# Kernel tuning notes

Measured on AMD Instinct MI355X. Metric: run time of the kernel, lower is better.

The kernel has to match this reference:

```python
import jax, jax.numpy as jnp
import numpy as np
from jax import lax

DIM = 256
NUM_HEADS = 8
HEAD_DIM = DIM // NUM_HEADS  # 32
SCALE = HEAD_DIM ** -0.5
KERNEL_SIZES = [5, 7, 9]
DILATIONS = [1, 2, 3]
# 'favor_small' allocation: weights ~ 1/k^2 over remain=num_heads-num_ranges=5
# -> extra=[3,2,0] -> heads_per_range = [4, 3, 1]
HEADS_PER_RANGE = [4, 3, 1]
B, H, W = 2, 64, 64


def setup_inputs() -> dict:
    key = jax.random.key(0)
    ks = jax.random.split(key, 9)
    d = {"x": jax.random.normal(ks[0], (B, DIM, H, W), jnp.float32)}
    for i in range(3):
        d[f"qkv_w{i}"] = jax.random.normal(ks[1 + 2 * i], (3 * DIM, DIM), jnp.float32) * 0.02
        d[f"qkv_b{i}"] = jnp.zeros((3 * DIM,), jnp.float32)
    d["proj_w"] = jax.random.normal(ks[7], (DIM, DIM), jnp.float32) * 0.02
    d["proj_b"] = jnp.zeros((DIM,), jnp.float32)
    return d


def _unfold(x, ksz, dil, h, hd):
    # x: (B, h*hd, H, W) -> (B, h, hd, L, H*W), zero-padded like F.unfold
    b, _, hh, ww = x.shape
    p = (ksz // 2) * dil
    patches = lax.conv_general_dilated_patches(
        x, (ksz, ksz), (1, 1), [(p, p), (p, p)], rhs_dilation=(dil, dil)
    )  # (B, h*hd*L, H, W), channel-major ordering matches F.unfold
    return patches.reshape(b, h, hd, ksz * ksz, hh * ww)


def _forward(x, qkv_params, proj_w, proj_b):
    b, c, hh, ww = x.shape
    hw = hh * ww
    outs = []
    hs = 0
    for i in range(len(KERNEL_SIZES)):
        w_i, b_i = qkv_params[i]
        # 1x1 conv -> qkv
        qkv = jnp.einsum('bchw,oc->bohw', x, w_i) + b_i[None, :, None, None]
        q, k, v = jnp.split(qkv, 3, axis=1)
        h_i = HEADS_PER_RANGE[i]
        he = hs + h_i
        # slice this range's heads
        q_r = q.reshape(b, NUM_HEADS, HEAD_DIM, hh, ww)[:, hs:he]
        k_r = k.reshape(b, NUM_HEADS, HEAD_DIM, hh, ww)[:, hs:he]
        v_r = v.reshape(b, NUM_HEADS, HEAD_DIM, hh, ww)[:, hs:he]
        ksz, dil = KERNEL_SIZES[i], DILATIONS[i]
        k_nb = _unfold(k_r.reshape(b, h_i * HEAD_DIM, hh, ww), ksz, dil, h_i, HEAD_DIM)
        v_nb = _unfold(v_r.reshape(b, h_i * HEAD_DIM, hh, ww), ksz, dil, h_i, HEAD_DIM)
        q_flat = q_r.reshape(b, h_i, HEAD_DIM, hw) * SCALE
        logits = jnp.einsum('bhdp,bhdlp->bhlp', q_flat, k_nb)  # (B, h_i, L, HW)
        attn = jax.nn.softmax(logits, axis=2)
        out_i = jnp.einsum('bhlp,bhdlp->bhdp', attn, v_nb)  # (B, h_i, d, HW)
        outs.append(out_i)
        hs = he
    out = jnp.concatenate(outs, axis=1).reshape(b, c, hh, ww)
    out = jnp.einsum('bchw,oc->bohw', out, proj_w) + proj_b[None, :, None, None]
    return out


def reference(x, qkv_w0, qkv_b0, qkv_w1, qkv_b1, qkv_w2, qkv_b2, proj_w, proj_b):
    qkv_params = [(qkv_w0, qkv_b0), (qkv_w1, qkv_b1), (qkv_w2, qkv_b2)]
    return _forward(x, qkv_params, proj_w, proj_b)
```

## Files before the change

kernel.cpp:

```cpp
#include <hip/hip_runtime.h>
#include <hip/hip_bf16.h>
#include <stdint.h>
#include <stddef.h>

typedef short bf16x8 __attribute__((ext_vector_type(8)));
typedef short s16x4 __attribute__((ext_vector_type(4)));
typedef float f32x4 __attribute__((ext_vector_type(4)));

#define HW 4096
#define WDIM 64

__device__ __forceinline__ short f2bf(float f) {
  union { __hip_bfloat16 b; short s; } u;
  u.b = __float2bfloat16(f);
  return u.s;
}
__device__ __forceinline__ float bf2f(short s) {
  union { unsigned u; float f; } u;
  u.u = ((unsigned)(unsigned short)s) << 16;
  return u.f;
}

__global__ void prep_weights(const float* __restrict__ w0, const float* __restrict__ w1,
                             const float* __restrict__ w2, const float* __restrict__ b0,
                             const float* __restrict__ b1, const float* __restrict__ b2,
                             const float* __restrict__ pw,
                             short* __restrict__ Wh, short* __restrict__ Wl,
                             short* __restrict__ Ph, short* __restrict__ Pl,
                             float* __restrict__ bias_sel) {
  int idx = blockIdx.x * 256 + threadIdx.x;
  if (idx < 768 * 256) {
    int j = idx >> 8;
    int h = (j & 255) >> 5;
    const float* w = (h < 4) ? w0 : ((h < 7) ? w1 : w2);
    float v = w[idx];
    short hi = f2bf(v);
    Wh[idx] = hi;
    Wl[idx] = f2bf(v - bf2f(hi));
  } else if (idx < 768 * 256 + 256 * 256) {
    int k = idx - 768 * 256;
    float v = pw[k];
    short hi = f2bf(v);
    Ph[k] = hi;
    Pl[k] = f2bf(v - bf2f(hi));
  } else if (idx < 768 * 256 + 256 * 256 + 768) {
    int j = idx - (768 * 256 + 256 * 256);
    int h = (j & 255) >> 5;
    const float* bb = (h < 4) ? b0 : ((h < 7) ? b1 : b2);
    bias_sel[j] = bb[j];
  }
}

__global__ void transpose_x(const float* __restrict__ x, short* __restrict__ XTh,
                            short* __restrict__ XTl) {
  __shared__ float tile[32][33];
  int b = blockIdx.z;
  int p0 = blockIdx.x * 32, c0 = blockIdx.y * 32;
  int tx = threadIdx.x, ty = threadIdx.y;
  const float* xb = x + (size_t)b * 256 * HW;
  #pragma unroll
  for (int i = 0; i < 32; i += 8)
    tile[ty + i][tx] = xb[(size_t)(c0 + ty + i) * HW + p0 + tx];
  __syncthreads();
  size_t ob = (size_t)b * HW * 256;
  #pragma unroll
  for (int i = 0; i < 32; i += 8) {
    float v = tile[tx][ty + i];
    short hi = f2bf(v);
    size_t o = ob + (size_t)(p0 + ty + i) * 256 + c0 + tx;
    XTh[o] = hi;
    XTl[o] = f2bf(v - bf2f(hi));
  }
}

template <int BM, int BN, int OUT>
__global__ __launch_bounds__(256) void gemm_split(
    const short* __restrict__ Ah, const short* __restrict__ Al,
    const short* __restrict__ Bh, const short* __restrict__ Bl,
    const float* __restrict__ bias, float* __restrict__ C, int M) {
  constexpr int LD = 40;
  constexpr int AL = BM / 64, BL = BN / 64;
  constexpr int WM = BM / 2, WN = BN / 2;
  constexpr int MR = WM / 16, NR = WN / 16;
  __shared__ short Ash[BM * LD], Asl[BM * LD], Bsh[BN * LD], Bsl[BN * LD];
  int tid = threadIdx.x;
  int b = blockIdx.z;
  size_t aoff = (size_t)blockIdx.y * BM * 256;
  size_t boff = (size_t)b * HW * 256 + (size_t)blockIdx.x * BN * 256;
  int lane = tid & 63, wid = tid >> 6;
  int wm = wid >> 1, wn = wid & 1;
  int il = lane & 15, kg = lane >> 4;
  f32x4 acc[MR][NR] = {};
  int row_s = tid >> 2;
  int kk_s = (tid & 3) * 8;

  for (int kt = 0; kt < 256; kt += 32) {
    bf16x8 rah[AL], ral[AL], rbh[BL], rbl[BL];
    #pragma unroll
    for (int i = 0; i < AL; ++i) {
      size_t g = aoff + (size_t)(row_s + 64 * i) * 256 + kt + kk_s;
      rah[i] = *(const bf16x8*)&Ah[g];
      ral[i] = *(const bf16x8*)&Al[g];
    }
    #pragma unroll
    for (int i = 0; i < BL; ++i) {
      size_t g = boff + (size_t)(row_s + 64 * i) * 256 + kt + kk_s;
      rbh[i] = *(const bf16x8*)&Bh[g];
      rbl[i] = *(const bf16x8*)&Bl[g];
    }
    __syncthreads();
    #pragma unroll
    for (int i = 0; i < AL; ++i) {
      *(bf16x8*)&Ash[(row_s + 64 * i) * LD + kk_s] = rah[i];
      *(bf16x8*)&Asl[(row_s + 64 * i) * LD + kk_s] = ral[i];
    }
    #pragma unroll
    for (int i = 0; i < BL; ++i) {
      *(bf16x8*)&Bsh[(row_s + 64 * i) * LD + kk_s] = rbh[i];
      *(bf16x8*)&Bsl[(row_s + 64 * i) * LD + kk_s] = rbl[i];
    }
    __syncthreads();
    bf16x8 afh[MR], afl[MR], bfh[NR], bfl[NR];
    #pragma unroll
    for (int mr = 0; mr < MR; ++mr) {
      int r = (wm * WM + mr * 16 + il) * LD + kg * 8;
      afh[mr] = *(bf16x8*)&Ash[r];
      afl[mr] = *(bf16x8*)&Asl[r];
    }
    #pragma unroll
    for (int nr = 0; nr < NR; ++nr) {
      int r = (wn * WN + nr * 16 + il) * LD + kg * 8;
      bfh[nr] = *(bf16x8*)&Bsh[r];
      bfl[nr] = *(bf16x8*)&Bsl[r];
    }
    #pragma unroll
    for (int mr = 0; mr < MR; ++mr)
      #pragma unroll
      for (int nr = 0; nr < NR; ++nr) {
        acc[mr][nr] = __builtin_amdgcn_mfma_f32_16x16x32_bf16(afh[mr], bfh[nr], acc[mr][nr], 0, 0, 0);
        acc[mr][nr] = __builtin_amdgcn_mfma_f32_16x16x32_bf16(afh[mr], bfl[nr], acc[mr][nr], 0, 0, 0);
        acc[mr][nr] = __builtin_amdgcn_mfma_f32_16x16x32_bf16(afl[mr], bfh[nr], acc[mr][nr], 0, 0, 0);
      }
  }

  int m0 = blockIdx.y * BM, n0 = blockIdx.x * BN;
  #pragma unroll
  for (int mr = 0; mr < MR; ++mr) {
    #pragma unroll
    for (int nr = 0; nr < NR; ++nr) {
      int grow0 = m0 + wm * WM + mr * 16 + kg * 4;
      int gcol = n0 + wn * WN + nr * 16 + il;
      if (OUT == 0) {
        int t = grow0 >> 8, h = (grow0 >> 5) & 7, d0 = grow0 & 31;
        size_t base = (((size_t)(b * 3 + t) * 8 + h) << 17) + ((size_t)gcol << 5) + d0;
        f32x4 vv;
        #pragma unroll
        for (int r = 0; r < 4; ++r) vv[r] = acc[mr][nr][r] + bias[grow0 + r];
        *(f32x4*)&C[base] = vv;
      } else {
        size_t cbase = (size_t)b * M * HW;
        #pragma unroll
        for (int r = 0; r < 4; ++r)
          C[cbase + (size_t)(grow0 + r) * HW + gcol] = acc[mr][nr][r] + bias[grow0 + r];
      }
    }
  }
}

template <int KSZ, int DIL>
__device__ __forceinline__ void attn_wave(const float* __restrict__ qkvt,
                                          short* __restrict__ Yh, short* __restrict__ Yl,
                                          int b, int hq, int p0, int lane) {
  constexpr int R = KSZ / 2;
  const float SCALE = 0.17677669529663687f;
  int pl = lane & 7;
  int dq = lane >> 3;
  int p = p0 + pl;
  const float* qp = qkvt + (((size_t)(b * 24 + hq)) << 17) + ((size_t)p << 5) + dq * 4;
  const float* kb = qkvt + (((size_t)(b * 24 + 8 + hq)) << 17) + dq * 4;
  const float* vb = qkvt + (((size_t)(b * 24 + 16 + hq)) << 17) + dq * 4;

  f32x4 q = *(const f32x4*)qp;
  #pragma unroll
  for (int j = 0; j < 4; ++j) q[j] *= SCALE;

  f32x4 acc = {0.f, 0.f, 0.f, 0.f};
  float denom = 0.f;
  int y = p >> 6, x = p & 63;

  #pragma unroll
  for (int dy = -R; dy <= R; ++dy) {
    #pragma unroll
    for (int dx = -R; dx <= R; ++dx) {
      int ny = y + dy * DIL;
      int nx = x + dx * DIL;
      bool valid = ((unsigned)ny < WDIM) & ((unsigned)nx < WDIM);
      int pp = valid ? (ny * WDIM + nx) : p;
      f32x4 kk = *(const f32x4*)(kb + ((size_t)pp << 5));
      f32x4 vv = *(const f32x4*)(vb + ((size_t)pp << 5));
      float s = q[0] * kk[0] + q[1] * kk[1] + q[2] * kk[2] + q[3] * kk[3];
      s += __shfl_xor(s, 8);
      s += __shfl_xor(s, 16);
      s += __shfl_xor(s, 32);
      float e = __expf(valid ? s : 0.0f);
      denom += e;
      float en = valid ? e : 0.0f;
      #pragma unroll
      for (int j = 0; j < 4; ++j) acc[j] += en * vv[j];
    }
  }

  float inv = 1.0f / denom;
  size_t yo = ((size_t)b * HW + p) * 256 + hq * 32 + dq * 4;
  s16x4 oh, ol;
  #pragma unroll
  for (int j = 0; j < 4; ++j) {
    float v = acc[j] * inv;
    short hi = f2bf(v);
    oh[j] = hi;
    ol[j] = f2bf(v - bf2f(hi));
  }
  *(s16x4*)&Yh[yo] = oh;
  *(s16x4*)&Yl[yo] = ol;
}

__global__ __launch_bounds__(256, 8) void attn_all(const float* __restrict__ qkvt,
                                                   short* __restrict__ Yh,
                                                   short* __restrict__ Yl) {
  int tid = threadIdx.x;
  int lane = tid & 63, wave = tid >> 6;
  int gw = blockIdx.x * 4 + wave;
  if (gw < 4096) {
    int tile = gw & 511;
    int t2 = gw >> 9;
    int b = t2 & 1, h = t2 >> 1;
    attn_wave<5, 1>(qkvt, Yh, Yl, b, h, tile * 8, lane);
  } else if (gw < 7168) {
    int s = gw - 4096;
    int tile = s & 511;
    int t2 = s >> 9;
    int b = t2 & 1, h = 4 + (t2 >> 1);
    attn_wave<7, 2>(qkvt, Yh, Yl, b, h, tile * 8, lane);
  } else {
    int s = gw - 7168;
    int tile = s & 511;
    int b = s >> 9;
    attn_wave<9, 3>(qkvt, Yh, Yl, b, 7, tile * 8, lane);
  }
}

extern "C" void kernel_launch(void* const* d_in, const int* in_sizes, int n_in,
                              void* d_out, int out_size, void* d_ws, size_t ws_size,
                              hipStream_t stream) {
  const float* x  = (const float*)d_in[0];
  const float* w0 = (const float*)d_in[1];
  const float* b0 = (const float*)d_in[2];
  const float* w1 = (const float*)d_in[3];
  const float* b1 = (const float*)d_in[4];
  const float* w2 = (const float*)d_in[5];
  const float* b2 = (const float*)d_in[6];
  const float* pw = (const float*)d_in[7];
  const float* pb = (const float*)d_in[8];

  char* ws = (char*)d_ws;
  float* qkvt = (float*)ws; ws += (size_t)2 * 768 * HW * 4;
  short* XTh = (short*)ws;  ws += (size_t)2 * HW * 256 * 2;
  short* XTl = (short*)ws;  ws += (size_t)2 * HW * 256 * 2;
  short* Yh  = (short*)ws;  ws += (size_t)2 * HW * 256 * 2;
  short* Yl  = (short*)ws;  ws += (size_t)2 * HW * 256 * 2;
  short* Wh  = (short*)ws;  ws += (size_t)768 * 256 * 2;
  short* Wl  = (short*)ws;  ws += (size_t)768 * 256 * 2;
  short* Ph  = (short*)ws;  ws += (size_t)256 * 256 * 2;
  short* Pl  = (short*)ws;  ws += (size_t)256 * 256 * 2;
  float* bsel= (float*)ws;  ws += 4096;

  prep_weights<<<1027, 256, 0, stream>>>(w0, w1, w2, b0, b1, b2, pw, Wh, Wl, Ph, Pl, bsel);
  transpose_x<<<dim3(128, 8, 2), dim3(32, 8), 0, stream>>>(x, XTh, XTl);
  gemm_split<64, 128, 0><<<dim3(32, 12, 2), 256, 0, stream>>>(Wh, Wl, XTh, XTl, bsel, qkvt, 768);
  attn_all<<<2048, 256, 0, stream>>>(qkvt, Yh, Yl);
  gemm_split<64, 64, 1><<<dim3(64, 4, 2), 256, 0, stream>>>(Ph, Pl, Yh, Yl, pb, (float*)d_out, 256);
}
```

Before: 198.0 us.

## Batch neighbor loads in groups of four and remap blocks to XCDs per head

The attention inner loop now issues the K/V loads for four neighbors before computing their scores and accumulating, so more memory requests are in flight per wave. Blocks are also remapped so that each XCD (blockIdx mod 8) handles the whole spatial range of one (batch, head) pair. Neighboring tiles of the same head then share that XCD's L2 cache. The cost is higher register pressure from holding four K/V vectors at once. The mapping assumes 2048 blocks and 8 XCDs, and leaves a stray unused label in the code.

After: 243.4 us. 23.0% more time.

```diff
diff --git a/kernel.cpp b/kernel.cpp
--- a/kernel.cpp
+++ b/kernel.cpp
@@ -172,6 +172,8 @@
                                           short* __restrict__ Yh, short* __restrict__ Yl,
                                           int b, int hq, int p0, int lane) {
   constexpr int R = KSZ / 2;
+  constexpr int L = KSZ * KSZ;
+  constexpr int NB = (L + 3) / 4;
   const float SCALE = 0.17677669529663687f;
   int pl = lane & 7;
   int dq = lane >> 3;
@@ -189,24 +191,45 @@
   int y = p >> 6, x = p & 63;
 
   #pragma unroll
-  for (int dy = -R; dy <= R; ++dy) {
-    #pragma unroll
-    for (int dx = -R; dx <= R; ++dx) {
-      int ny = y + dy * DIL;
-      int nx = x + dx * DIL;
-      bool valid = ((unsigned)ny < WDIM) & ((unsigned)nx < WDIM);
-      int pp = valid ? (ny * WDIM + nx) : p;
-      f32x4 kk = *(const f32x4*)(kb + ((size_t)pp << 5));
-      f32x4 vv = *(const f32x4*)(vb + ((size_t)pp << 5));
-      float s = q[0] * kk[0] + q[1] * kk[1] + q[2] * kk[2] + q[3] * kk[3];
-      s += __shfl_xor(s, 8);
-      s += __shfl_xor(s, 16);
-      s += __shfl_xor(s, 32);
-      float e = __expf(valid ? s : 0.0f);
-      denom += e;
-      float en = valid ? e : 0.0f;
-      #pragma unroll
-      for (int j = 0; j < 4; ++j) acc[j] += en * vv[j];
+  for (int g = 0; g < NB; ++g) {
+    f32x4 kk[4], vv[4];
+    bool val[4];
+    #pragma unroll
+    for (int j = 0; j < 4; ++j) {
+      constexpr_helper:;
+      const int i = 0;
+      (void)i;
+      int vi = g * 4 + j;
+      if (vi < L) {
+        int dy = vi / KSZ - R, dx = vi % KSZ - R;
+        int ny = y + dy * DIL, nx = x + dx * DIL;
+        val[j] = (((unsigned)ny < WDIM) & ((unsigned)nx < WDIM));
+        int pp = val[j] ? (ny * WDIM + nx) : p;
+        kk[j] = *(const f32x4*)(kb + ((size_t)pp << 5));
+        vv[j] = *(const f32x4*)(vb + ((size_t)pp << 5));
+      }
+    }
+    float e[4];
+    #pragma unroll
+    for (int j = 0; j < 4; ++j) {
+      int vi = g * 4 + j;
+      if (vi < L) {
+        float s = q[0] * kk[j][0] + q[1] * kk[j][1] + q[2] * kk[j][2] + q[3] * kk[j][3];
+        s += __shfl_xor(s, 8);
+        s += __shfl_xor(s, 16);
+        s += __shfl_xor(s, 32);
+        e[j] = __expf(val[j] ? s : 0.0f);
+        denom += e[j];
+      }
+    }
+    #pragma unroll
+    for (int j = 0; j < 4; ++j) {
+      int vi = g * 4 + j;
+      if (vi < L) {
+        float en = val[j] ? e[j] : 0.0f;
+        #pragma unroll
+        for (int k = 0; k < 4; ++k) acc[k] += en * vv[j][k];
+      }
     }
   }
 
@@ -229,23 +252,23 @@
                                                    short* __restrict__ Yl) {
   int tid = threadIdx.x;
   int lane = tid & 63, wave = tid >> 6;
-  int gw = blockIdx.x * 4 + wave;
-  if (gw < 4096) {
-    int tile = gw & 511;
-    int t2 = gw >> 9;
-    int b = t2 & 1, h = t2 >> 1;
-    attn_wave<5, 1>(qkvt, Yh, Yl, b, h, tile * 8, lane);
-  } else if (gw < 7168) {
-    int s = gw - 4096;
-    int tile = s & 511;
-    int t2 = s >> 9;
-    int b = t2 & 1, h = 4 + (t2 >> 1);
-    attn_wave<7, 2>(qkvt, Yh, Yl, b, h, tile * 8, lane);
+  int bid = blockIdx.x;
+  int xcd = bid & 7;
+  int idx = bid >> 3;
+  int half = idx >> 7;
+  int tile = idx & 127;
+  int c = xcd + 8 * half;
+  int p0 = tile * 32 + wave * 8;
+  if (c < 8) {
+    int h = c >> 1, b = c & 1;
+    attn_wave<5, 1>(qkvt, Yh, Yl, b, h, p0, lane);
+  } else if (c < 14) {
+    int s = c - 8;
+    int h = 4 + (s >> 1), b = s & 1;
+    attn_wave<7, 2>(qkvt, Yh, Yl, b, h, p0, lane);
   } else {
-    int s = gw - 7168;
-    int tile = s & 511;
-    int b = s >> 9;
-    attn_wave<9, 3>(qkvt, Yh, Yl, b, 7, tile * 8, lane);
+    int b = c & 1;
+    attn_wave<9, 3>(qkvt, Yh, Yl, b, 7, p0, lane);
   }
 }
 
```

## Software-pipeline neighbor K/V loads in groups of four with double buffering

Applied to the files above, without the earlier changes.

The per-neighbor attention loop becomes a double-buffered pipeline. Each step loads K/V for the next four neighbors while it computes dot products, shuffles and exp for the current four, and the independent shuffle chains are interleaved. Launch bounds are relaxed from 8 to 4 blocks per CU to leave room for the extra registers. This targets global-load latency stalls, at the cost of higher register pressure and lower occupancy.

Result: slower. 205.6 us (+3.8%).

```diff
diff --git a/kernel.cpp b/kernel.cpp
--- a/kernel.cpp
+++ b/kernel.cpp
@@ -167,11 +167,67 @@
   }
 }
 
+
+template <int KSZ, int DIL, int L>
+__device__ __forceinline__ void loadg(int g, f32x4 (&kk)[4], f32x4 (&vv)[4], bool (&vm)[4],
+                                      const float* __restrict__ kb,
+                                      const float* __restrict__ vb,
+                                      int y, int x, int p) {
+  constexpr int R = KSZ / 2;
+  #pragma unroll
+  for (int j = 0; j < 4; ++j) {
+    int vi = g * 4 + j;
+    if (vi < L) {
+      int dy = vi / KSZ - R, dx = vi % KSZ - R;
+      int ny = y + dy * DIL, nx = x + dx * DIL;
+      bool val = (((unsigned)ny < WDIM) & ((unsigned)nx < WDIM));
+      vm[j] = val;
+      int pp = val ? (ny * WDIM + nx) : p;
+      kk[j] = *(const f32x4*)(kb + ((size_t)pp << 5));
+      vv[j] = *(const f32x4*)(vb + ((size_t)pp << 5));
+    }
+  }
+}
+
+template <int L>
+__device__ __forceinline__ void compg(int g, const f32x4 (&kk)[4], const f32x4 (&vv)[4],
+                                      const bool (&vm)[4], const f32x4& q,
+                                      f32x4& acc, float& denom) {
+  float s[4], t[4];
+  #pragma unroll
+  for (int j = 0; j < 4; ++j)
+    if (g * 4 + j < L)
+      s[j] = q[0] * kk[j][0] + q[1] * kk[j][1] + q[2] * kk[j][2] + q[3] * kk[j][3];
+  #pragma unroll
+  for (int j = 0; j < 4; ++j) if (g * 4 + j < L) t[j] = __shfl_xor(s[j], 8);
+  #pragma unroll
+  for (int j = 0; j < 4; ++j) if (g * 4 + j < L) s[j] += t[j];
+  #pragma unroll
+  for (int j = 0; j < 4; ++j) if (g * 4 + j < L) t[j] = __shfl_xor(s[j], 16);
+  #pragma unroll
+  for (int j = 0; j < 4; ++j) if (g * 4 + j < L) s[j] += t[j];
+  #pragma unroll
+  for (int j = 0; j < 4; ++j) if (g * 4 + j < L) t[j] = __shfl_xor(s[j], 32);
+  #pragma unroll
+  for (int j = 0; j < 4; ++j) if (g * 4 + j < L) s[j] += t[j];
+  #pragma unroll
+  for (int j = 0; j < 4; ++j) {
+    if (g * 4 + j < L) {
+      float e = __expf(vm[j] ? s[j] : 0.0f);
+      denom += e;
+      float en = vm[j] ? e : 0.0f;
+      #pragma unroll
+      for (int k2 = 0; k2 < 4; ++k2) acc[k2] += en * vv[j][k2];
+    }
+  }
+}
+
 template <int KSZ, int DIL>
 __device__ __forceinline__ void attn_wave(const float* __restrict__ qkvt,
                                           short* __restrict__ Yh, short* __restrict__ Yl,
                                           int b, int hq, int p0, int lane) {
-  constexpr int R = KSZ / 2;
+  constexpr int L = KSZ * KSZ;
+  constexpr int NB = (L + 3) / 4;
   const float SCALE = 0.17677669529663687f;
   int pl = lane & 7;
   int dq = lane >> 3;
@@ -188,25 +244,17 @@
   float denom = 0.f;
   int y = p >> 6, x = p & 63;
 
-  #pragma unroll
-  for (int dy = -R; dy <= R; ++dy) {
-    #pragma unroll
-    for (int dx = -R; dx <= R; ++dx) {
-      int ny = y + dy * DIL;
-      int nx = x + dx * DIL;
-      bool valid = ((unsigned)ny < WDIM) & ((unsigned)nx < WDIM);
-      int pp = valid ? (ny * WDIM + nx) : p;
-      f32x4 kk = *(const f32x4*)(kb + ((size_t)pp << 5));
-      f32x4 vv = *(const f32x4*)(vb + ((size_t)pp << 5));
-      float s = q[0] * kk[0] + q[1] * kk[1] + q[2] * kk[2] + q[3] * kk[3];
-      s += __shfl_xor(s, 8);
-      s += __shfl_xor(s, 16);
-      s += __shfl_xor(s, 32);
-      float e = __expf(valid ? s : 0.0f);
-      denom += e;
-      float en = valid ? e : 0.0f;
-      #pragma unroll
-      for (int j = 0; j < 4; ++j) acc[j] += en * vv[j];
+  f32x4 kA[4], vA[4]; bool mA[4];
+  f32x4 kB[4], vB[4]; bool mB[4];
+  loadg<KSZ, DIL, L>(0, kA, vA, mA, kb, vb, y, x, p);
+  #pragma unroll
+  for (int g = 0; g < NB; ++g) {
+    if ((g & 1) == 0) {
+      if (g + 1 < NB) loadg<KSZ, DIL, L>(g + 1, kB, vB, mB, kb, vb, y, x, p);
+      compg<L>(g, kA, vA, mA, q, acc, denom);
+    } else {
+      if (g + 1 < NB) loadg<KSZ, DIL, L>(g + 1, kA, vA, mA, kb, vb, y, x, p);
+      compg<L>(g, kB, vB, mB, q, acc, denom);
     }
   }
 
@@ -224,7 +272,7 @@
   *(s16x4*)&Yl[yo] = ol;
 }
 
-__global__ __launch_bounds__(256, 8) void attn_all(const float* __restrict__ qkvt,
+__global__ __launch_bounds__(256, 4) void attn_all(const float* __restrict__ qkvt,
                                                    short* __restrict__ Yh,
                                                    short* __restrict__ Yl) {
   int tid = threadIdx.x;
```
